# Kernel tuning notes

Hardware: AMD Instinct MI355X
Metric: run time of the kernel (lower is better)

The kernel has to match this reference:

```python
import jax, jax.numpy as jnp
import numpy as np

B, T, H = 4, 2048, 2048


def setup_inputs() -> dict:
    key = jax.random.key(0)
    ks = jax.random.split(key, 10)
    s = 0.02  # weight init scale
    return {
        "hidden": jax.random.normal(ks[0], (B, T, H), jnp.float32),
        "time_decay": jax.random.normal(ks[1], (H,), jnp.float32),
        "time_first": jax.random.normal(ks[2], (H,), jnp.float32),
        "time_mix_key": jax.random.uniform(ks[3], (1, 1, H), jnp.float32),
        "time_mix_value": jax.random.uniform(ks[4], (1, 1, H), jnp.float32),
        "time_mix_receptance": jax.random.uniform(ks[5], (1, 1, H), jnp.float32),
        "Wk": jax.random.normal(ks[6], (H, H), jnp.float32) * s,
        "Wv": jax.random.normal(ks[7], (H, H), jnp.float32) * s,
        "Wr": jax.random.normal(ks[8], (H, H), jnp.float32) * s,
        "Wo": jax.random.normal(ks[9], (H, H), jnp.float32) * s,
    }


def _wkv(time_decay, time_first, k, v):
    # k, v: [B, T, D]. Log-sum-exp stabilized RWKV WKV recurrence via lax.scan.
    td = -jnp.exp(time_decay.astype(jnp.float32))  # [D]
    tf = time_first.astype(jnp.float32)            # [D]
    kT = jnp.swapaxes(k, 0, 1).astype(jnp.float32)  # [T, B, D]
    vT = jnp.swapaxes(v, 0, 1).astype(jnp.float32)
    bd = (k.shape[0], k.shape[2])
    init = (jnp.zeros(bd, jnp.float32),               # num_state
            jnp.zeros(bd, jnp.float32),               # den_state
            jnp.full(bd, -1e38, jnp.float32))         # max_state

    def step(carry, kv_t):
        num, den, mx = carry
        kt, vt = kv_t
        # output for this step
        mfo = jnp.maximum(mx, kt + tf)
        e1 = jnp.exp(mx - mfo)
        e2 = jnp.exp(kt + tf - mfo)
        out = (e1 * num + e2 * vt) / (e1 * den + e2)
        # state update with decay
        mfs = jnp.maximum(mx + td, kt)
        e1s = jnp.exp(mx + td - mfs)
        e2s = jnp.exp(kt - mfs)
        return (e1s * num + e2s * vt, e1s * den + e2s, mfs), out

    _, outT = jax.lax.scan(step, init, (kT, vT))  # [T, B, D]
    return jnp.swapaxes(outT, 0, 1).astype(k.dtype)


def reference(hidden, time_decay, time_first, time_mix_key, time_mix_value,
              time_mix_receptance, Wk, Wv, Wr, Wo):
    # time-shift: shifted[:, t] = hidden[:, t-1], zero at t=0
    shifted = jnp.pad(hidden, ((0, 0), (1, 0), (0, 0)))[:, :-1]
    key = hidden * time_mix_key + shifted * (1.0 - time_mix_key)
    value = hidden * time_mix_value + shifted * (1.0 - time_mix_value)
    rec = hidden * time_mix_receptance + shifted * (1.0 - time_mix_receptance)
    k = key @ Wk
    v = value @ Wv
    r = jax.nn.sigmoid(rec @ Wr)
    rwkv = _wkv(time_decay, time_first, k, v)
    return (r * rwkv) @ Wo
```

## Files before the change

kernel.cpp:

```cpp
#include <hip/hip_runtime.h>
#include <hip/hip_bf16.h>
#include <stdint.h>


typedef short short8 __attribute__((ext_vector_type(8)));
typedef float f32x4 __attribute__((ext_vector_type(4)));

#define WKV_C 32

__device__ __forceinline__ void gld_lds16(const void* gptr, void* lptr) {
  void* g = const_cast<void*>(gptr);
  __builtin_amdgcn_global_load_lds(
      (__attribute__((address_space(1))) void*)g,
      (__attribute__((address_space(3))) void*)lptr, 16, 0, 0);
}

__device__ __forceinline__ unsigned short f2bf(float f) {
  __bf16 b = (__bf16)f;
  return __builtin_bit_cast(unsigned short, b);
}
__device__ __forceinline__ unsigned short f2h(float f) {
  _Float16 h = (_Float16)f;
  return __builtin_bit_cast(unsigned short, h);
}
__device__ __forceinline__ float h2f(unsigned short u) {
  return (float)__builtin_bit_cast(_Float16, u);
}

__global__ void transpose_cast(const float* __restrict__ W,
                               unsigned short* __restrict__ WT, int n) {
  __shared__ float tile[32][33];
  const int tx = threadIdx.x, ty = threadIdx.y;
  const int x = blockIdx.x * 32 + tx;
#pragma unroll
  for (int j = 0; j < 32; j += 8) {
    int row = blockIdx.y * 32 + ty + j;
    tile[ty + j][tx] = W[(size_t)row * n + x];
  }
  __syncthreads();
#pragma unroll
  for (int j = 0; j < 32; j += 8) {
    int orow = blockIdx.x * 32 + ty + j;
    int ocol = blockIdx.y * 32 + tx;
    WT[(size_t)orow * n + ocol] = f2bf(tile[tx][ty + j]);
  }
}

__global__ void mix3_kernel(const float4* __restrict__ hid,
                            const float4* __restrict__ mk4,
                            const float4* __restrict__ mv4,
                            const float4* __restrict__ mr4,
                            ushort4* __restrict__ xk, ushort4* __restrict__ xv,
                            ushort4* __restrict__ xr, int T, int H4) {
  size_t idx = (size_t)blockIdx.x * blockDim.x + threadIdx.x;
  int c4 = (int)(idx % H4);
  int t = (int)(idx / H4) % T;
  float4 h = hid[idx];
  float4 p = make_float4(0.f, 0.f, 0.f, 0.f);
  if (t != 0) p = hid[idx - H4];
  float4 mk = mk4[c4], mv = mv4[c4], mr = mr4[c4];
  ushort4 ok, ov, orr;
  ok.x = f2bf(h.x * mk.x + p.x * (1.f - mk.x));
  ok.y = f2bf(h.y * mk.y + p.y * (1.f - mk.y));
  ok.z = f2bf(h.z * mk.z + p.z * (1.f - mk.z));
  ok.w = f2bf(h.w * mk.w + p.w * (1.f - mk.w));
  ov.x = f2bf(h.x * mv.x + p.x * (1.f - mv.x));
  ov.y = f2bf(h.y * mv.y + p.y * (1.f - mv.y));
  ov.z = f2bf(h.z * mv.z + p.z * (1.f - mv.z));
  ov.w = f2bf(h.w * mv.w + p.w * (1.f - mv.w));
  orr.x = f2bf(h.x * mr.x + p.x * (1.f - mr.x));
  orr.y = f2bf(h.y * mr.y + p.y * (1.f - mr.y));
  orr.z = f2bf(h.z * mr.z + p.z * (1.f - mr.z));
  orr.w = f2bf(h.w * mr.w + p.w * (1.f - mr.w));
  xk[idx] = ok;
  xv[idx] = ov;
  xr[idx] = orr;
}

#define MODE_F32 0
#define MODE_F16 1
#define MODE_F16_SIG 2

#define GK 2048
#define GN 2048

#define STAGE_A(kt_, u, b)                                                     \
  {                                                                            \
    _Pragma("unroll") for (int s_ = 0; s_ < 2; ++s_)                           \
        gld_lds16(Ab + (s_ * 128 + (u) * 64) * GK + (kt_) * 64,                \
                  ldsT + (b) * 16384 + (s_ * 128 + (u) * 64) * 64);            \
  }
#define STAGE_B(kt_, u, b)                                                     \
  {                                                                            \
    _Pragma("unroll") for (int s_ = 0; s_ < 2; ++s_)                           \
        gld_lds16(Bb + (s_ * 128 + (u) * 32) * GK + (kt_) * 64,                \
                  ldsT + 32768 + (b) * 16384 + ((u) * 128 + s_ * 64) * 64);    \
  }

#define LOAD_A(b, qi)                                                          \
  {                                                                            \
    _Pragma("unroll") for (int ip_ = 0; ip_ < 4; ++ip_) {                      \
      aF[ip_][0] =                                                             \
          *(const short8*)(pA0 + (b) * 16384 + (qi) * 4096 + ip_ * 1024);      \
      aF[ip_][1] =                                                             \
          *(const short8*)(pA1 + (b) * 16384 + (qi) * 4096 + ip_ * 1024);      \
    }                                                                          \
  }
#define LOAD_B(b, qj, dst)                                                     \
  {                                                                            \
    _Pragma("unroll") for (int jj_ = 0; jj_ < 2; ++jj_) {                      \
      dst[jj_][0] =                                                            \
          *(const short8*)(pB0 + (b) * 16384 + (qj) * 8192 + jj_ * 1024);      \
      dst[jj_][1] =                                                            \
          *(const short8*)(pB1 + (b) * 16384 + (qj) * 8192 + jj_ * 1024);      \
    }                                                                          \
  }

#define MFMA16(qi, qj, bfr)                                                    \
  {                                                                            \
    _Pragma("unroll") for (int ip_ = 0; ip_ < 4; ++ip_)                        \
        _Pragma("unroll") for (int jj_ = 0; jj_ < 2; ++jj_) {                  \
      acc[(qi) * 4 + ip_][(qj) * 2 + jj_] =                                    \
          __builtin_amdgcn_mfma_f32_16x16x32_bf16(                             \
              aF[ip_][0], bfr[jj_][0], acc[(qi) * 4 + ip_][(qj) * 2 + jj_],    \
              0, 0, 0);                                                        \
      acc[(qi) * 4 + ip_][(qj) * 2 + jj_] =                                    \
          __builtin_amdgcn_mfma_f32_16x16x32_bf16(                             \
              aF[ip_][1], bfr[jj_][1], acc[(qi) * 4 + ip_][(qj) * 2 + jj_],    \
              0, 0, 0);                                                        \
    }                                                                          \
  }

#define PHASE(b, qi, qj, STG, WAITN)                                           \
  {                                                                            \
    STG;                                                                       \
    if ((qi) == 0 && (qj) == 0) { LOAD_A(b, 0); LOAD_B(b, 0, bF0); }           \
    if ((qi) == 0 && (qj) == 1) { LOAD_B(b, 1, bF1); }                         \
    if ((qi) == 1 && (qj) == 0) { LOAD_A(b, 1); }                              \
    __builtin_amdgcn_s_barrier();                                              \
    if ((WAITN) == 6) asm volatile("s_waitcnt vmcnt(6)" ::: "memory");         \
    if ((WAITN) == 0) asm volatile("s_waitcnt vmcnt(0)" ::: "memory");         \
    __builtin_amdgcn_s_setprio(1);                                             \
    if ((qj) == 0) { MFMA16(qi, 0, bF0); } else { MFMA16(qi, 1, bF1); }        \
    __builtin_amdgcn_s_setprio(0);                                             \
    asm volatile("s_waitcnt lgkmcnt(0)" ::: "memory");                         \
    __builtin_amdgcn_s_barrier();                                              \
  }

#define ITER(kt, LAST)                                                         \
  {                                                                            \
    PHASE(0, 0, 0, STAGE_A((kt) + 1, 1, 1), -1);                               \
    PHASE(0, 0, 1, if (!(LAST)) STAGE_A((kt) + 2, 0, 0), -1);                  \
    PHASE(0, 1, 0, if (!(LAST)) STAGE_B((kt) + 2, 0, 0), -1);                  \
    PHASE(0, 1, 1, if (!(LAST)) STAGE_B((kt) + 2, 1, 0), (LAST) ? 0 : 6);      \
    PHASE(1, 0, 0, if (!(LAST)) STAGE_A((kt) + 2, 1, 0), -1);                  \
    PHASE(1, 0, 1, if (!(LAST)) STAGE_A((kt) + 3, 0, 1), -1);                  \
    PHASE(1, 1, 0, if (!(LAST)) STAGE_B((kt) + 3, 0, 1), -1);                  \
    PHASE(1, 1, 1, if (!(LAST)) STAGE_B((kt) + 3, 1, 1), (LAST) ? -1 : 6);     \
  }

template <int MODE>
__global__ __launch_bounds__(512, 2) void gemm_bt(
    const unsigned short* __restrict__ A, const unsigned short* __restrict__ Bt,
    void* __restrict__ Cv) {
  __shared__ unsigned short ldsm[65536];

  const int t = threadIdx.x;
  const int lane = t & 63;
  const int wave = t >> 6;
  const int wm = wave >> 2;
  const int wn = wave & 3;
  const int quad = lane >> 4;
  const int lm = lane & 15;
  const int sw = lm & 7;

  const int lin = blockIdx.y * 8 + blockIdx.x;
  const int cls = lin & 7;
  const int q = lin >> 3;
  const int mTile = cls * 4 + (q & 3);
  const int nTile = q >> 2;
  const size_t mBase = (size_t)mTile * 256;
  const size_t nBase = (size_t)nTile * 256;

  const int lr = t >> 3;
  const int swz = (t & 7) ^ (lr & 7);
  const unsigned short* Ab = A + mBase * GK + lr * GK + swz * 8;
  const unsigned short* Bb =
      Bt + nBase * GK + (lr >> 5) * 64 * GK + (lr & 31) * GK + swz * 8;
  unsigned short* ldsT = ldsm + t * 8;

  const unsigned short* pA0 = ldsm + (wm * 128 + lm) * 64 + ((0 + quad) ^ sw) * 8;
  const unsigned short* pA1 = ldsm + (wm * 128 + lm) * 64 + ((4 + quad) ^ sw) * 8;
  const unsigned short* pB0 =
      ldsm + 32768 + (wn * 32 + lm) * 64 + ((0 + quad) ^ sw) * 8;
  const unsigned short* pB1 =
      ldsm + 32768 + (wn * 32 + lm) * 64 + ((4 + quad) ^ sw) * 8;

  short8 aF[4][2];
  short8 bF0[2][2];
  short8 bF1[2][2];
  f32x4 acc[8][4];
#pragma unroll
  for (int i = 0; i < 8; ++i)
#pragma unroll
    for (int j = 0; j < 4; ++j) {
      f32x4 zz = {0.f, 0.f, 0.f, 0.f};
      acc[i][j] = zz;
    }

  STAGE_A(0, 0, 0);
  STAGE_B(0, 0, 0);
  STAGE_B(0, 1, 0);
  STAGE_A(0, 1, 0);
  STAGE_A(1, 0, 1);
  STAGE_B(1, 0, 1);
  STAGE_B(1, 1, 1);
  asm volatile("s_waitcnt vmcnt(6)" ::: "memory");
  __builtin_amdgcn_s_barrier();

  const int KT = GK >> 6;
  int kt = 0;
#pragma unroll 1
  for (; kt + 2 < KT; kt += 2) { ITER(kt, 0); }
  ITER(kt, 1);

#pragma unroll
  for (int i = 0; i < 8; ++i) {
    const size_t row = mBase + wm * 128 + (i >> 2) * 64 + (i & 3) * 16 + quad * 4;
#pragma unroll
    for (int j = 0; j < 4; ++j) {
      const size_t col = nBase + wn * 64 + (j >> 1) * 32 + (j & 1) * 16 + lm;
#pragma unroll
      for (int rg = 0; rg < 4; ++rg) {
        float x = acc[i][j][rg];
        size_t off = (row + rg) * GN + col;
        if (MODE == MODE_F32) {
          ((float*)Cv)[off] = x;
        } else {
          if (MODE == MODE_F16_SIG) x = 1.0f / (1.0f + __expf(-x));
          ((unsigned short*)Cv)[off] = f2h(x);
        }
      }
    }
  }
}

__global__ void wkv_pass1(const unsigned short* __restrict__ kk,
                          const unsigned short* __restrict__ vv,
                          const float* __restrict__ tdec,
                          float* __restrict__ pn, float* __restrict__ pd,
                          float* __restrict__ pm, int T, int H, int L) {
  int idx = blockIdx.x * blockDim.x + threadIdx.x;
  int h = idx % H;
  int bc = idx / H;
  int c = bc % WKV_C;
  int b = bc / WKV_C;
  const float td = -__expf(tdec[h]);
  size_t base = ((size_t)b * T + (size_t)c * L) * H + h;
  const unsigned short* kp = kk + base;
  const unsigned short* vp = vv + base;
  float num = 0.f, den = 0.f, mx = -1e38f;
#pragma unroll 8
  for (int t = 0; t < L; ++t) {
    float kt = h2f(kp[(size_t)t * H]);
    float vt = h2f(vp[(size_t)t * H]);
    float mtd = mx + td;
    float mfs = fmaxf(mtd, kt);
    float e1s = __expf(mtd - mfs);
    float e2s = __expf(kt - mfs);
    num = e1s * num + e2s * vt;
    den = e1s * den + e2s;
    mx = mfs;
  }
  pn[idx] = num;
  pd[idx] = den;
  pm[idx] = mx;
}

__global__ void wkv_pass2(const float* __restrict__ pn,
                          const float* __restrict__ pd,
                          const float* __restrict__ pm,
                          const float* __restrict__ tdec,
                          float* __restrict__ sn, float* __restrict__ sd,
                          float* __restrict__ sm, int H, int L) {
  int idx = blockIdx.x * blockDim.x + threadIdx.x;
  int h = idx % H;
  int b = idx / H;
  const float Ltd = -__expf(tdec[h]) * (float)L;
  float num = 0.f, den = 0.f, mx = -1e38f;
#pragma unroll
  for (int c = 0; c < WKV_C; ++c) {
    size_t o = ((size_t)b * WKV_C + c) * H + h;
    sn[o] = num;
    sd[o] = den;
    sm[o] = mx;
    float mtd = mx + Ltd;
    float cm = pm[o];
    float mnew = fmaxf(mtd, cm);
    float e1 = __expf(mtd - mnew);
    float e2 = __expf(cm - mnew);
    num = e1 * num + e2 * pn[o];
    den = e1 * den + e2 * pd[o];
    mx = mnew;
  }
}

__global__ void wkv_pass3(const unsigned short* __restrict__ kk,
                          const unsigned short* __restrict__ vv,
                          const unsigned short* rr,
                          const float* __restrict__ sn,
                          const float* __restrict__ sd,
                          const float* __restrict__ sm,
                          const float* __restrict__ tdec,
                          const float* __restrict__ tfir, unsigned short* y,
                          int T, int H, int L) {
  int idx = blockIdx.x * blockDim.x + threadIdx.x;
  int h = idx % H;
  int bc = idx / H;
  int c = bc % WKV_C;
  int b = bc / WKV_C;
  const float td = -__expf(tdec[h]);
  const float tf = tfir[h];
  float num = sn[idx], den = sd[idx], mx = sm[idx];
  size_t base = ((size_t)b * T + (size_t)c * L) * H + h;
  const unsigned short* kp = kk + base;
  const unsigned short* vp = vv + base;
  const unsigned short* rp = rr + base;
  unsigned short* yp = y + base;
#pragma unroll 4
  for (int t = 0; t < L; ++t) {
    size_t o = (size_t)t * H;
    float kt = h2f(kp[o]);
    float vt = h2f(vp[o]);
    float rt = h2f(rp[o]);
    float ktf = kt + tf;
    float mfo = fmaxf(mx, ktf);
    float e1 = __expf(mx - mfo);
    float e2 = __expf(ktf - mfo);
    float out = __fdividef(e1 * num + e2 * vt, e1 * den + e2);
    yp[o] = f2bf(rt * out);
    float mtd = mx + td;
    float mfs = fmaxf(mtd, kt);
    float e1s = __expf(mtd - mfs);
    float e2s = __expf(kt - mfs);
    num = e1s * num + e2s * vt;
    den = e1s * den + e2s;
    mx = mfs;
  }
}

extern "C" void kernel_launch(void* const* d_in, const int* in_sizes, int n_in,
                              void* d_out, int out_size, void* d_ws,
                              size_t ws_size, hipStream_t stream) {
  const int Bb = 4, T = 2048, H = 2048;
  const int M = Bb * T;
  const int L = T / WKV_C;

  const float* hidden = (const float*)d_in[0];
  const float* time_decay = (const float*)d_in[1];
  const float* time_first = (const float*)d_in[2];
  const float* tmk = (const float*)d_in[3];
  const float* tmv = (const float*)d_in[4];
  const float* tmr = (const float*)d_in[5];
  const float* Wk = (const float*)d_in[6];
  const float* Wv = (const float*)d_in[7];
  const float* Wr = (const float*)d_in[8];
  const float* Wo = (const float*)d_in[9];
  float* out = (float*)d_out;

  const size_t szWT = (size_t)H * H * 2;
  const size_t szMH = (size_t)M * H * 2;
  const size_t need = szWT + 4 * szMH + 1024;
  if (ws_size < need) return;

  char* ws = (char*)d_ws;
  size_t off = 0;
  auto alloc = [&](size_t bytes) {
    char* p = ws + off;
    off += (bytes + 255) & ~(size_t)255;
    return p;
  };
  unsigned short* WT = (unsigned short*)alloc(szWT);
  unsigned short* A1 = (unsigned short*)alloc(szMH);
  unsigned short* A2 = (unsigned short*)alloc(szMH);
  unsigned short* A3 = (unsigned short*)alloc(szMH);
  unsigned short* A4 = (unsigned short*)alloc(szMH);

  unsigned short* xk = A1;
  unsigned short* xv = A2;
  unsigned short* xr = A3;
  unsigned short* kbuf = A4;
  unsigned short* vbuf = A1;
  unsigned short* rbuf = A2;

  const size_t nCH = (size_t)Bb * WKV_C * H;
  float* pn = (float*)A3;
  float* pd = pn + nCH;
  float* pm = pd + nCH;
  float* sn = pm + nCH;
  float* sd = sn + nCH;
  float* sm = sd + nCH;

  const dim3 txG(H / 32, H / 32), txB(32, 8);
  const int H4 = H / 4;
  const dim3 gmG(H / 256, M / 256), gmB(512);

  mix3_kernel<<<dim3((M * H4) / 256), dim3(256), 0, stream>>>(
      (const float4*)hidden, (const float4*)tmk, (const float4*)tmv,
      (const float4*)tmr, (ushort4*)xk, (ushort4*)xv, (ushort4*)xr, T, H4);

  transpose_cast<<<txG, txB, 0, stream>>>(Wk, WT, H);
  gemm_bt<MODE_F16><<<gmG, gmB, 0, stream>>>(xk, WT, kbuf);
  transpose_cast<<<txG, txB, 0, stream>>>(Wv, WT, H);
  gemm_bt<MODE_F16><<<gmG, gmB, 0, stream>>>(xv, WT, vbuf);
  transpose_cast<<<txG, txB, 0, stream>>>(Wr, WT, H);
  gemm_bt<MODE_F16_SIG><<<gmG, gmB, 0, stream>>>(xr, WT, rbuf);

  const int nThreads1 = Bb * WKV_C * H;
  wkv_pass1<<<dim3(nThreads1 / 256), dim3(256), 0, stream>>>(
      kbuf, vbuf, time_decay, pn, pd, pm, T, H, L);
  wkv_pass2<<<dim3((Bb * H) / 256), dim3(256), 0, stream>>>(
      pn, pd, pm, time_decay, sn, sd, sm, H, L);
  wkv_pass3<<<dim3(nThreads1 / 256), dim3(256), 0, stream>>>(
      kbuf, vbuf, rbuf, sn, sd, sm, time_decay, time_first, rbuf, T, H, L);

  transpose_cast<<<txG, txB, 0, stream>>>(Wo, WT, H);
  gemm_bt<MODE_F32><<<gmG, gmB, 0, stream>>>(rbuf, WT, out);
}
```

Measured before the change: 486.4 us.

## Prefetch GEMM LDS fragments a phase ahead and fold WKV pass2 into pass3

The GEMM main loop now issues the LDS fragment reads for the next phase right after the current phase's MFMAs, using partial lgkmcnt waits. The intent is to hide LDS read latency behind the barrier instead of loading fragments at the start of each phase and draining to zero. Separately, the WKV chunk-prefix kernel (pass2) is removed. Each pass3 thread now recomputes its chunk's starting state from the per-chunk partials, which saves a launch and the state buffers at the cost of redundant serial work (up to 31 steps per thread).

```diff
diff --git a/kernel.cpp b/kernel.cpp
--- a/kernel.cpp
+++ b/kernel.cpp
@@ -97,7 +97,7 @@
                   ldsT + 32768 + (b) * 16384 + ((u) * 128 + s_ * 64) * 64);    \
   }
 
-#define LOAD_A(b, qi)                                                          \
+#define PRE_A(b, qi)                                                           \
   {                                                                            \
     _Pragma("unroll") for (int ip_ = 0; ip_ < 4; ++ip_) {                      \
       aF[ip_][0] =                                                             \
@@ -106,15 +106,25 @@
           *(const short8*)(pA1 + (b) * 16384 + (qi) * 4096 + ip_ * 1024);      \
     }                                                                          \
   }
-#define LOAD_B(b, qj, dst)                                                     \
+#define PRE_B0(b)                                                              \
   {                                                                            \
     _Pragma("unroll") for (int jj_ = 0; jj_ < 2; ++jj_) {                      \
-      dst[jj_][0] =                                                            \
-          *(const short8*)(pB0 + (b) * 16384 + (qj) * 8192 + jj_ * 1024);      \
-      dst[jj_][1] =                                                            \
-          *(const short8*)(pB1 + (b) * 16384 + (qj) * 8192 + jj_ * 1024);      \
+      bF0[jj_][0] = *(const short8*)(pB0 + (b) * 16384 + jj_ * 1024);          \
+      bF0[jj_][1] = *(const short8*)(pB1 + (b) * 16384 + jj_ * 1024);          \
     }                                                                          \
   }
+#define PRE_B1(b)                                                              \
+  {                                                                            \
+    _Pragma("unroll") for (int jj_ = 0; jj_ < 2; ++jj_) {                      \
+      bF1[jj_][0] = *(const short8*)(pB0 + (b) * 16384 + 8192 + jj_ * 1024);   \
+      bF1[jj_][1] = *(const short8*)(pB1 + (b) * 16384 + 8192 + jj_ * 1024);   \
+    }                                                                          \
+  }
+
+#define FENCE0 asm volatile("s_waitcnt lgkmcnt(0)" ::: "memory")
+#define FENCE4 asm volatile("s_waitcnt lgkmcnt(4)" ::: "memory")
+#define FENCE8 asm volatile("s_waitcnt lgkmcnt(8)" ::: "memory")
+#define FENCE12 asm volatile("s_waitcnt lgkmcnt(12)" ::: "memory")
 
 #define MFMA16(qi, qj, bfr)                                                    \
   {                                                                            \
@@ -131,32 +141,35 @@
     }                                                                          \
   }
 
-#define PHASE(b, qi, qj, STG, WAITN)                                           \
+#define PH(qi, qj, STG, PRE, FEN, WAITN)                                       \
   {                                                                            \
     STG;                                                                       \
-    if ((qi) == 0 && (qj) == 0) { LOAD_A(b, 0); LOAD_B(b, 0, bF0); }           \
-    if ((qi) == 0 && (qj) == 1) { LOAD_B(b, 1, bF1); }                         \
-    if ((qi) == 1 && (qj) == 0) { LOAD_A(b, 1); }                              \
     __builtin_amdgcn_s_barrier();                                              \
     if ((WAITN) == 6) asm volatile("s_waitcnt vmcnt(6)" ::: "memory");         \
     if ((WAITN) == 0) asm volatile("s_waitcnt vmcnt(0)" ::: "memory");         \
     __builtin_amdgcn_s_setprio(1);                                             \
     if ((qj) == 0) { MFMA16(qi, 0, bF0); } else { MFMA16(qi, 1, bF1); }        \
     __builtin_amdgcn_s_setprio(0);                                             \
-    asm volatile("s_waitcnt lgkmcnt(0)" ::: "memory");                         \
+    PRE;                                                                       \
+    FEN;                                                                       \
     __builtin_amdgcn_s_barrier();                                              \
   }
 
 #define ITER(kt, LAST)                                                         \
   {                                                                            \
-    PHASE(0, 0, 0, STAGE_A((kt) + 1, 1, 1), -1);                               \
-    PHASE(0, 0, 1, if (!(LAST)) STAGE_A((kt) + 2, 0, 0), -1);                  \
-    PHASE(0, 1, 0, if (!(LAST)) STAGE_B((kt) + 2, 0, 0), -1);                  \
-    PHASE(0, 1, 1, if (!(LAST)) STAGE_B((kt) + 2, 1, 0), (LAST) ? 0 : 6);      \
-    PHASE(1, 0, 0, if (!(LAST)) STAGE_A((kt) + 2, 1, 0), -1);                  \
-    PHASE(1, 0, 1, if (!(LAST)) STAGE_A((kt) + 3, 0, 1), -1);                  \
-    PHASE(1, 1, 0, if (!(LAST)) STAGE_B((kt) + 3, 0, 1), -1);                  \
-    PHASE(1, 1, 1, if (!(LAST)) STAGE_B((kt) + 3, 1, 1), (LAST) ? -1 : 6);     \
+    PH(0, 0, STAGE_A((kt) + 1, 1, 1), PRE_B1(0), FENCE4, -1);                  \
+    PH(0, 1, if (!(LAST)) STAGE_A((kt) + 2, 0, 0), PRE_A(0, 1), FENCE8, -1);   \
+    PH(1, 0, if (!(LAST)) STAGE_B((kt) + 2, 0, 0), {}, FENCE0, -1);            \
+    PH(1, 1, if (!(LAST)) STAGE_B((kt) + 2, 1, 0), PRE_A(1, 0); PRE_B0(1),     \
+       FENCE12, (LAST) ? 0 : 6);                                               \
+    PH(0, 0, if (!(LAST)) STAGE_A((kt) + 2, 1, 0), PRE_B1(1), FENCE4, -1);     \
+    PH(0, 1, if (!(LAST)) STAGE_A((kt) + 3, 0, 1), PRE_A(1, 1), FENCE8, -1);   \
+    PH(1, 0, if (!(LAST)) STAGE_B((kt) + 3, 0, 1), {}, FENCE0, -1);            \
+    if (!(LAST)) {                                                             \
+      PH(1, 1, STAGE_B((kt) + 3, 1, 1), PRE_A(0, 0); PRE_B0(0), FENCE12, 6);   \
+    } else {                                                                   \
+      PH(1, 1, {}, {}, FENCE0, -1);                                            \
+    }                                                                          \
   }
 
 template <int MODE>
@@ -217,6 +230,8 @@
   STAGE_B(1, 1, 1);
   asm volatile("s_waitcnt vmcnt(6)" ::: "memory");
   __builtin_amdgcn_s_barrier();
+  PRE_A(0, 0);
+  PRE_B0(0);
 
   const int KT = GK >> 6;
   int kt = 0;
@@ -277,40 +292,12 @@
   pm[idx] = mx;
 }
 
-__global__ void wkv_pass2(const float* __restrict__ pn,
-                          const float* __restrict__ pd,
-                          const float* __restrict__ pm,
-                          const float* __restrict__ tdec,
-                          float* __restrict__ sn, float* __restrict__ sd,
-                          float* __restrict__ sm, int H, int L) {
-  int idx = blockIdx.x * blockDim.x + threadIdx.x;
-  int h = idx % H;
-  int b = idx / H;
-  const float Ltd = -__expf(tdec[h]) * (float)L;
-  float num = 0.f, den = 0.f, mx = -1e38f;
-#pragma unroll
-  for (int c = 0; c < WKV_C; ++c) {
-    size_t o = ((size_t)b * WKV_C + c) * H + h;
-    sn[o] = num;
-    sd[o] = den;
-    sm[o] = mx;
-    float mtd = mx + Ltd;
-    float cm = pm[o];
-    float mnew = fmaxf(mtd, cm);
-    float e1 = __expf(mtd - mnew);
-    float e2 = __expf(cm - mnew);
-    num = e1 * num + e2 * pn[o];
-    den = e1 * den + e2 * pd[o];
-    mx = mnew;
-  }
-}
-
 __global__ void wkv_pass3(const unsigned short* __restrict__ kk,
                           const unsigned short* __restrict__ vv,
                           const unsigned short* rr,
-                          const float* __restrict__ sn,
-                          const float* __restrict__ sd,
-                          const float* __restrict__ sm,
+                          const float* __restrict__ pn,
+                          const float* __restrict__ pd,
+                          const float* __restrict__ pm,
                           const float* __restrict__ tdec,
                           const float* __restrict__ tfir, unsigned short* y,
                           int T, int H, int L) {
@@ -321,7 +308,19 @@
   int b = bc / WKV_C;
   const float td = -__expf(tdec[h]);
   const float tf = tfir[h];
-  float num = sn[idx], den = sd[idx], mx = sm[idx];
+  const float Ltd = td * (float)L;
+  float num = 0.f, den = 0.f, mx = -1e38f;
+  for (int cp = 0; cp < c; ++cp) {
+    size_t o = ((size_t)b * WKV_C + cp) * H + h;
+    float mtd = mx + Ltd;
+    float cm = pm[o];
+    float mnew = fmaxf(mtd, cm);
+    float e1 = __expf(mtd - mnew);
+    float e2 = __expf(cm - mnew);
+    num = e1 * num + e2 * pn[o];
+    den = e1 * den + e2 * pd[o];
+    mx = mnew;
+  }
   size_t base = ((size_t)b * T + (size_t)c * L) * H + h;
   const unsigned short* kp = kk + base;
   const unsigned short* vp = vv + base;
@@ -397,9 +396,6 @@
   float* pn = (float*)A3;
   float* pd = pn + nCH;
   float* pm = pd + nCH;
-  float* sn = pm + nCH;
-  float* sd = sn + nCH;
-  float* sm = sd + nCH;
 
   const dim3 txG(H / 32, H / 32), txB(32, 8);
   const int H4 = H / 4;
@@ -419,10 +415,8 @@
   const int nThreads1 = Bb * WKV_C * H;
   wkv_pass1<<<dim3(nThreads1 / 256), dim3(256), 0, stream>>>(
       kbuf, vbuf, time_decay, pn, pd, pm, T, H, L);
-  wkv_pass2<<<dim3((Bb * H) / 256), dim3(256), 0, stream>>>(
-      pn, pd, pm, time_decay, sn, sd, sm, H, L);
   wkv_pass3<<<dim3(nThreads1 / 256), dim3(256), 0, stream>>>(
-      kbuf, vbuf, rbuf, sn, sd, sm, time_decay, time_first, rbuf, T, H, L);
+      kbuf, vbuf, rbuf, pn, pd, pm, time_decay, time_first, rbuf, T, H, L);
 
   transpose_cast<<<txG, txB, 0, stream>>>(Wo, WT, H);
   gemm_bt<MODE_F32><<<gmG, gmB, 0, stream>>>(rbuf, WT, out);
```

Measured after the change: 490.0 us. Within noise of the previous version (+0.7%).

## Drop mid-phase GEMM barrier and fold WKV chunk-prefix pass into pass3

Applied to the files above, without the earlier changes.

Inside the GEMM phase macro, the global-to-LDS staging call now comes after the LDS fragment loads, and the barrier that sat between them is removed, leaving one barrier per phase. Separately, the wkv_pass2 kernel is deleted and each pass3 thread recomputes its own chunk-prefix state by scanning the preceding chunk summaries. This removes a kernel launch and the write/read of the intermediate state buffers, at the cost of redundant serial prefix work (up to 31 steps) per thread. Dropping the barrier risks LDS races if the staging writes overlap buffers still being read by other waves.

```diff
diff --git a/kernel.cpp b/kernel.cpp
--- a/kernel.cpp
+++ b/kernel.cpp
@@ -133,11 +133,10 @@
 
 #define PHASE(b, qi, qj, STG, WAITN)                                           \
   {                                                                            \
-    STG;                                                                       \
     if ((qi) == 0 && (qj) == 0) { LOAD_A(b, 0); LOAD_B(b, 0, bF0); }           \
     if ((qi) == 0 && (qj) == 1) { LOAD_B(b, 1, bF1); }                         \
     if ((qi) == 1 && (qj) == 0) { LOAD_A(b, 1); }                              \
-    __builtin_amdgcn_s_barrier();                                              \
+    STG;                                                                       \
     if ((WAITN) == 6) asm volatile("s_waitcnt vmcnt(6)" ::: "memory");         \
     if ((WAITN) == 0) asm volatile("s_waitcnt vmcnt(0)" ::: "memory");         \
     __builtin_amdgcn_s_setprio(1);                                             \
@@ -277,40 +276,12 @@
   pm[idx] = mx;
 }
 
-__global__ void wkv_pass2(const float* __restrict__ pn,
-                          const float* __restrict__ pd,
-                          const float* __restrict__ pm,
-                          const float* __restrict__ tdec,
-                          float* __restrict__ sn, float* __restrict__ sd,
-                          float* __restrict__ sm, int H, int L) {
-  int idx = blockIdx.x * blockDim.x + threadIdx.x;
-  int h = idx % H;
-  int b = idx / H;
-  const float Ltd = -__expf(tdec[h]) * (float)L;
-  float num = 0.f, den = 0.f, mx = -1e38f;
-#pragma unroll
-  for (int c = 0; c < WKV_C; ++c) {
-    size_t o = ((size_t)b * WKV_C + c) * H + h;
-    sn[o] = num;
-    sd[o] = den;
-    sm[o] = mx;
-    float mtd = mx + Ltd;
-    float cm = pm[o];
-    float mnew = fmaxf(mtd, cm);
-    float e1 = __expf(mtd - mnew);
-    float e2 = __expf(cm - mnew);
-    num = e1 * num + e2 * pn[o];
-    den = e1 * den + e2 * pd[o];
-    mx = mnew;
-  }
-}
-
 __global__ void wkv_pass3(const unsigned short* __restrict__ kk,
                           const unsigned short* __restrict__ vv,
                           const unsigned short* rr,
-                          const float* __restrict__ sn,
-                          const float* __restrict__ sd,
-                          const float* __restrict__ sm,
+                          const float* __restrict__ pn,
+                          const float* __restrict__ pd,
+                          const float* __restrict__ pm,
                           const float* __restrict__ tdec,
                           const float* __restrict__ tfir, unsigned short* y,
                           int T, int H, int L) {
@@ -321,7 +292,19 @@
   int b = bc / WKV_C;
   const float td = -__expf(tdec[h]);
   const float tf = tfir[h];
-  float num = sn[idx], den = sd[idx], mx = sm[idx];
+  const float Ltd = td * (float)L;
+  float num = 0.f, den = 0.f, mx = -1e38f;
+  for (int cp = 0; cp < c; ++cp) {
+    size_t o = ((size_t)b * WKV_C + cp) * H + h;
+    float mtd = mx + Ltd;
+    float cm = pm[o];
+    float mnew = fmaxf(mtd, cm);
+    float e1 = __expf(mtd - mnew);
+    float e2 = __expf(cm - mnew);
+    num = e1 * num + e2 * pn[o];
+    den = e1 * den + e2 * pd[o];
+    mx = mnew;
+  }
   size_t base = ((size_t)b * T + (size_t)c * L) * H + h;
   const unsigned short* kp = kk + base;
   const unsigned short* vp = vv + base;
@@ -397,9 +380,6 @@
   float* pn = (float*)A3;
   float* pd = pn + nCH;
   float* pm = pd + nCH;
-  float* sn = pm + nCH;
-  float* sd = sn + nCH;
-  float* sm = sd + nCH;
 
   const dim3 txG(H / 32, H / 32), txB(32, 8);
   const int H4 = H / 4;
@@ -419,10 +399,8 @@
   const int nThreads1 = Bb * WKV_C * H;
   wkv_pass1<<<dim3(nThreads1 / 256), dim3(256), 0, stream>>>(
       kbuf, vbuf, time_decay, pn, pd, pm, T, H, L);
-  wkv_pass2<<<dim3((Bb * H) / 256), dim3(256), 0, stream>>>(
-      pn, pd, pm, time_decay, sn, sd, sm, H, L);
   wkv_pass3<<<dim3(nThreads1 / 256), dim3(256), 0, stream>>>(
-      kbuf, vbuf, rbuf, sn, sd, sm, time_decay, time_first, rbuf, T, H, L);
+      kbuf, vbuf, rbuf, pn, pd, pm, time_decay, time_first, rbuf, T, H, L);
 
   transpose_cast<<<txG, txB, 0, stream>>>(Wo, WT, H);
   gemm_bt<MODE_F32><<<gmG, gmB, 0, stream>>>(rbuf, WT, out);
```

Measured after the change: 486.3 us. No clear change (-0.0%).
